# Performance work log

Hardware: AMD Instinct MI355X
Metric: run time of the kernel (lower is better)

The kernel has to match this reference:

```python
import jax, jax.numpy as jnp
import numpy as np

MIN_, MAX_, KSZ, IGNORE_IDX = 10, 10, 3, -255
B, H, W = 256, 256, 256
LI_MAX_ITERS = 64


def setup_inputs() -> dict:
    key = jax.random.key(0)
    x = jax.random.uniform(key, (B, 1, H, W), dtype=jnp.float32)
    return {"x": x}


def _otsu(hist):
    # hist: [256] counts. Returns Otsu threshold (bin value); fg = img > t.
    bins = jnp.arange(256, dtype=jnp.float32)
    w0 = jnp.cumsum(hist)[:-1]
    w1 = hist.sum() - w0
    s0 = jnp.cumsum(hist * bins)[:-1]
    s_tot = (hist * bins).sum()
    m0 = s0 / jnp.maximum(w0, 1e-12)
    m1 = (s_tot - s0) / jnp.maximum(w1, 1e-12)
    var_b = w0 * w1 * (m0 - m1) ** 2
    return jnp.argmax(var_b).astype(jnp.float32)


def _li(hist, init_t):
    # Histogram-based Li iterative minimum cross-entropy threshold
    # (skimage.filters.threshold_li with initial_guess=init_t).
    bins = jnp.arange(256, dtype=jnp.float32)
    img_min = jnp.min(jnp.where(hist > 0, bins, 255.0))
    vals = bins - img_min  # shift so values >= 0 (as skimage does)
    csum = jnp.cumsum(hist)
    cvsum = jnp.cumsum(hist * vals)
    n_tot, s_tot = csum[-1], cvsum[-1]
    tol = 0.5  # integer image -> half the minimal value spacing

    def body(state):
        t_curr, _, i = state
        # background: img <= t_curr + img_min
        idx = jnp.clip(jnp.floor(t_curr + img_min).astype(jnp.int32), 0, 255)
        n_back, s_back = csum[idx], cvsum[idx]
        n_fore, s_fore = n_tot - n_back, s_tot - s_back
        mean_back = jnp.where(n_back > 0, s_back / jnp.maximum(n_back, 1.0), 0.0)
        mean_fore = s_fore / jnp.maximum(n_fore, 1.0)
        eps = 1e-12
        t_next = (mean_back - mean_fore) / (
            jnp.log(jnp.maximum(mean_back, eps)) - jnp.log(jnp.maximum(mean_fore, eps)))
        t_next = jnp.where(mean_back < eps, mean_fore / 2.0, t_next)
        return (t_next, t_curr, i + 1)

    def cond(state):
        t_curr, t_prev, i = state
        return (jnp.abs(t_curr - t_prev) > tol) & (i < LI_MAX_ITERS)

    t0 = init_t - img_min
    t_fin, _, _ = jax.lax.while_loop(cond, body, (t0, t0 + 10.0, 0))
    return t_fin + img_min


def _sample_mask(key, region, k):
    # Uniform sampling without replacement of up to k pixels from region
    # (bool [H,W]) via random-score top-k (equiv. to torch.multinomial
    # with uniform probs, w/o replacement).
    flat = region.reshape(-1)
    scores = jnp.where(flat, jax.random.uniform(key, (flat.shape[0],)), -1.0)
    top, idx = jax.lax.top_k(scores, k)
    valid = (top >= 0.0).astype(jnp.int32)
    mask = jnp.zeros(flat.shape[0], jnp.int32).at[idx].max(valid)
    return mask.reshape(region.shape)


def _dilate(m):
    # kornia dilation with ones (KSZ,KSZ) kernel on a 0/1 mask == max filter.
    return jax.lax.reduce_window(m, 0, jax.lax.max, (KSZ, KSZ), (1, 1), "SAME")


def _per_image(img_u8, key_fg, key_bg):
    # img_u8: [H,W] int32 in [0,255]
    hist = jnp.zeros(256, jnp.float32).at[img_u8.ravel()].add(1.0)
    otsu = jnp.clip(_otsu(hist), 1.0, 254.0)  # clamp 0->1, 255->254
    li_t = _li(hist, otsu)
    roi = img_u8.astype(jnp.float32) > li_t

    fg = _sample_mask(key_fg, roi, MAX_)
    bg = _sample_mask(key_bg, jnp.logical_not(roi), MIN_)
    if KSZ > 1:
        fg = _dilate(fg)
        bg = _dilate(bg)

    overlap = (fg + bg) == 2
    fg = jnp.where(overlap, 0, fg)
    bg = jnp.where(overlap, 0, bg)

    seeds = jnp.full((H, W), IGNORE_IDX, jnp.int32)
    seeds = jnp.where(bg == 1, 0, seeds)
    seeds = jnp.where(fg == 1, 1, seeds)
    return seeds


def reference(x):
    b = x.shape[0]
    # (cam*255).astype(uint8): truncation, cam in [0,1]
    img = jnp.clip(jnp.floor(x[:, 0] * 255.0), 0, 255).astype(jnp.int32)
    keys = jax.random.split(jax.random.key(1), (b, 2))
    return jax.vmap(_per_image)(img, keys[:, 0], keys[:, 1])
```

## Files before the change

kernel.cpp:

```cpp
#include <hip/hip_runtime.h>
#include <stdint.h>

#define NPIX 65536
#define IGN (-255)
#define CAP 1022
#define META_LI   2048
#define META_CF   2049
#define META_CB   2050
#define META_NROI 2051
#define META_FG   2052
#define META_BG   3074

__device__ __forceinline__ uint32_t rotl32(uint32_t v, uint32_t r){ return (v<<r)|(v>>(32u-r)); }

__device__ __forceinline__ void tf2x32(uint32_t k0, uint32_t k1, uint32_t x0, uint32_t x1,
                                       uint32_t &o0, uint32_t &o1){
  uint32_t k2 = k0 ^ k1 ^ 0x1BD11BDAu;
  x0 += k0; x1 += k1;
#define TFR(r) { x0 += x1; x1 = rotl32(x1,(r)); x1 ^= x0; }
  TFR(13u) TFR(15u) TFR(26u) TFR(6u)   x0 += k1; x1 += k2 + 1u;
  TFR(17u) TFR(29u) TFR(16u) TFR(24u)  x0 += k2; x1 += k0 + 2u;
  TFR(13u) TFR(15u) TFR(26u) TFR(6u)   x0 += k0; x1 += k1 + 3u;
  TFR(17u) TFR(29u) TFR(16u) TFR(24u)  x0 += k1; x1 += k2 + 4u;
  TFR(13u) TFR(15u) TFR(26u) TFR(6u)   x0 += k2; x1 += k0 + 5u;
#undef TFR
  o0 = x0; o1 = x1;
}

__device__ __forceinline__ unsigned long long packCand(uint32_t bits, uint32_t pix){
  float f = __uint_as_float((bits >> 9) | 0x3f800000u) - 1.0f;
  uint32_t u = __float_as_uint(f) ^ 0x80000000u;
  return ((unsigned long long)u << 32) | (unsigned long long)(0xFFFFFFFFu - pix);
}

__device__ __forceinline__ void t10_insert(unsigned long long* l, unsigned long long c){
  if (c > l[9]) {
    l[9] = c;
#pragma unroll
    for (int i = 9; i > 0; --i){
      unsigned long long a = l[i-1], b2 = l[i];
      if (b2 > a){ l[i-1] = b2; l[i] = a; }
    }
  }
}

__global__ __launch_bounds__(256, 8)
void ka_hist_fill(const float* __restrict__ x, int* __restrict__ out){
  const int blk = blockIdx.x;
  const int b = blk >> 3, j8 = blk & 7;
  const int tid = threadIdx.x;
  const float4* x4 = (const float4*)(x + (size_t)b * NPIX) + j8 * 2048;
  int4* o4 = (int4*)(out + (size_t)b * NPIX) + j8 * 2048;

  __shared__ uint32_t histR[1024];
#pragma unroll
  for (int k = 0; k < 4; ++k) histR[tid + 256*k] = 0u;
  __syncthreads();

  const int4 f4 = make_int4(IGN, IGN, IGN, IGN);
  const uint32_t c4 = (uint32_t)(tid & 3);
#pragma unroll
  for (int jj = 0; jj < 8; ++jj){
    int p4 = tid + 256*jj;
    float4 v = x4[p4];
    if (j8 != 0 || jj >= 4) o4[p4] = f4;
    uint32_t u0 = (uint32_t)min(max((int)floorf(v.x*255.0f),0),255);
    uint32_t u1 = (uint32_t)min(max((int)floorf(v.y*255.0f),0),255);
    uint32_t u2 = (uint32_t)min(max((int)floorf(v.z*255.0f),0),255);
    uint32_t u3 = (uint32_t)min(max((int)floorf(v.w*255.0f),0),255);
    atomicAdd(&histR[(u0<<2)|c4],1u); atomicAdd(&histR[(u1<<2)|c4],1u);
    atomicAdd(&histR[(u2<<2)|c4],1u); atomicAdd(&histR[(u3<<2)|c4],1u);
  }
  __syncthreads();
  uint32_t s = histR[4*tid] + histR[4*tid+1] + histR[4*tid+2] + histR[4*tid+3];
  out[(size_t)b*NPIX + j8*256 + tid] = (int)s;
}

__global__ __launch_bounds__(256, 2)
void kb_thresh(int* __restrict__ out){
  const int b = blockIdx.x;
  const int tid = threadIdx.x;
  int* meta = out + (size_t)b * NPIX;

  __shared__ float csum[256], cvsum[256];
  __shared__ int s_imin;
  __shared__ unsigned long long s_best;
  if (tid == 0){ s_imin = 255; s_best = 0ull; }
  __syncthreads();

  int h = 0;
#pragma unroll
  for (int j = 0; j < 8; ++j) h += meta[j*256 + tid];
  if (h) atomicMin(&s_imin, tid);
  __syncthreads();
  const float img_min = (float)s_imin;

  csum[tid]  = (float)h;
  cvsum[tid] = (float)h * ((float)tid - img_min);
  __syncthreads();
  for (int off = 1; off < 256; off <<= 1){
    float a = 0.f, c2 = 0.f;
    if (tid >= off){ a = csum[tid-off]; c2 = cvsum[tid-off]; }
    __syncthreads();
    if (tid >= off){ csum[tid] += a; cvsum[tid] += c2; }
    __syncthreads();
  }

  {
    float s_tot_o = cvsum[255] + img_min * csum[255];
    if (tid < 255){
      float w0 = csum[tid];
      float w1 = 65536.0f - w0;
      float cs = cvsum[tid] + img_min * csum[tid];
      float m0 = cs / fmaxf(w0, 1e-12f);
      float m1 = (s_tot_o - cs) / fmaxf(w1, 1e-12f);
      float d = m0 - m1;
      float vb = (w0*w1) * (d*d);
      unsigned long long pk =
        ((unsigned long long)__float_as_uint(vb) << 32) | (unsigned long long)(255 - tid);
      atomicMax(&s_best, pk);
    }
  }
  __syncthreads();

  if (tid == 0){
    int bestIdx = 255 - (int)(s_best & 0xFFFFFFFFull);
    float otsu = fminf(fmaxf((float)bestIdx, 1.0f), 254.0f);
    float n_tot = csum[255], s_tot = cvsum[255];
    float t_curr = otsu - img_min, t_prev = t_curr + 10.0f;
    int it = 0;
    while (fabsf(t_curr - t_prev) > 0.5f && it < 64){
      int idx = min(max((int)floorf(t_curr + img_min), 0), 255);
      float n_back = csum[idx], s_back = cvsum[idx];
      float n_fore = n_tot - n_back, s_fore = s_tot - s_back;
      float mean_back = (n_back > 0.0f) ? (s_back / fmaxf(n_back, 1.0f)) : 0.0f;
      float mean_fore = s_fore / fmaxf(n_fore, 1.0f);
      float t_next = (mean_back - mean_fore) /
                     (logf(fmaxf(mean_back, 1e-12f)) - logf(fmaxf(mean_fore, 1e-12f)));
      if (mean_back < 1e-12f) t_next = mean_fore * 0.5f;
      t_prev = t_curr; t_curr = t_next; ++it;
    }
    float lit = t_curr + img_min;
    meta[META_LI] = __float_as_int(lit);
    int idx = min(max((int)floorf(lit), 0), 255);
    meta[META_NROI] = NPIX - (int)csum[idx];
    meta[META_CF] = 0;
    meta[META_CB] = 0;
  }
}

__global__ __launch_bounds__(256, 4)
void kc_score(const float* __restrict__ x, int* __restrict__ out){
  const int blk = blockIdx.x;
  const int b = blk >> 3, j8 = blk & 7;
  const int tid = threadIdx.x;
  int* meta = out + (size_t)b * NPIX;
  const float4* x4 = (const float4*)(x + (size_t)b * NPIX) + j8 * 2048;

  __shared__ uint32_t s_kw[4];
  __shared__ float s_lit;
  if (tid < 2){
    uint32_t o0, o1;
    tf2x32(0u, 1u, 0u, (uint32_t)(2*b + tid), o0, o1);
    s_kw[2*tid] = o0; s_kw[2*tid+1] = o1;
  }
  if (tid == 0) s_lit = __int_as_float(meta[META_LI]);
  __syncthreads();

  const float lit = s_lit;
  const uint32_t fk0 = s_kw[0], fk1 = s_kw[1], bk0 = s_kw[2], bk1 = s_kw[3];
  const uint32_t THRM = (0xFF000000u >> 9);
#pragma unroll
  for (int jj = 0; jj < 8; ++jj){
    int p4 = tid + 256*jj;
    float4 v = x4[p4];
    uint32_t u0 = (uint32_t)min(max((int)floorf(v.x*255.0f),0),255);
    uint32_t u1 = (uint32_t)min(max((int)floorf(v.y*255.0f),0),255);
    uint32_t u2 = (uint32_t)min(max((int)floorf(v.z*255.0f),0),255);
    uint32_t u3 = (uint32_t)min(max((int)floorf(v.w*255.0f),0),255);
    uint32_t pk = u0 | (u1<<8) | (u2<<16) | (u3<<24);
    uint32_t pix0 = (uint32_t)(j8*8192 + 4*p4);
#pragma unroll
    for (int s = 0; s < 4; ++s){
      uint32_t q = (pk >> (8*s)) & 255u;
      bool r = ((float)q > lit);
      uint32_t o0, o1;
      tf2x32(r ? fk0 : bk0, r ? fk1 : bk1, 0u, pix0 + (uint32_t)s, o0, o1);
      uint32_t bits = o0 ^ o1;
      if ((bits >> 9) >= THRM){
        int r2 = r ? 0 : 1;
        int idx = atomicAdd(&meta[META_CF + r2], 1);
        if (idx < CAP) meta[(r2 ? META_BG : META_FG) + idx] = (int)(pix0 + (uint32_t)s);
      }
    }
  }
}

__global__ __launch_bounds__(1024, 4)
void kd_final(const float* __restrict__ x, int* __restrict__ out){
  const int b = blockIdx.x;
  const int tid = threadIdx.x;
  int* meta = out + (size_t)b * NPIX;
  int* outb = meta;
  const float* img = x + (size_t)b * NPIX;

  __shared__ unsigned long long buf[2][CAP];
  __shared__ uint32_t s_kw[4];
  __shared__ int s_cnt[2], s_fail[2], s_np[2];
  __shared__ float s_lit;
  __shared__ int s_pr[2][10], s_pc[2][10];

  if (tid < 2){
    uint32_t o0, o1;
    tf2x32(0u, 1u, 0u, (uint32_t)(2*b + tid), o0, o1);
    s_kw[2*tid] = o0; s_kw[2*tid+1] = o1;
  }
  if (tid == 0){
    s_lit = __int_as_float(meta[META_LI]);
    int c0 = meta[META_CF], c1 = meta[META_CB];
    int nroi = meta[META_NROI];
    s_cnt[0] = c0; s_cnt[1] = c1;
    int m0r = nroi, m1r = NPIX - nroi;
    s_fail[0] = (c0 > CAP) || (c0 < 10 && c0 != m0r);
    s_fail[1] = (c1 > CAP) || (c1 < 10 && c1 != m1r);
  }
  __syncthreads();

  {
    int r2 = tid >> 9, lane = tid & 511;
    uint32_t kk0 = s_kw[2*r2], kk1 = s_kw[2*r2+1];
    int n = min(s_cnt[r2], CAP);
    for (int i = lane; i < n; i += 512){
      uint32_t pix = (uint32_t)meta[(r2 ? META_BG : META_FG) + i];
      uint32_t o0, o1; tf2x32(kk0, kk1, 0u, pix, o0, o1);
      buf[r2][i] = packCand(o0 ^ o1, pix);
    }
  }
  __syncthreads();

  const float lit = s_lit;
  if (s_fail[0] || s_fail[1]){
    if (tid < 64){
      for (int r2 = 0; r2 < 2; ++r2){
        if (!s_fail[r2]) continue;
        uint32_t kk0 = s_kw[2*r2], kk1 = s_kw[2*r2+1];
        unsigned long long t[10];
#pragma unroll
        for (int i = 0; i < 10; ++i) t[i] = 0ull;
        for (int k2 = 0; k2 < 1024; ++k2){
          uint32_t pix = (uint32_t)(tid + 64*k2);
          float v = img[pix];
          int q = min(max((int)floorf(v*255.0f),0),255);
          bool r = ((float)q > lit);
          if (r != (r2 == 0)) continue;
          uint32_t o0, o1; tf2x32(kk0, kk1, 0u, pix, o0, o1);
          t10_insert(t, packCand(o0 ^ o1, pix));
        }
#pragma unroll
        for (int i = 0; i < 10; ++i) buf[r2][tid*10 + i] = t[i];
      }
    }
    __syncthreads();
    if (tid < 2 && s_fail[tid]){
      unsigned long long t[10];
#pragma unroll
      for (int i = 0; i < 10; ++i) t[i] = 0ull;
      for (int i = 0; i < 640; ++i) t10_insert(t, buf[tid][i]);
#pragma unroll
      for (int i = 0; i < 10; ++i) buf[tid][i] = t[i];
      s_cnt[tid] = 10;
    }
    __syncthreads();
  }

  if (tid == 0 || tid == 64){
    int r2 = (tid == 0) ? 0 : 1;
    int n = min(s_cnt[r2], CAP);
    unsigned long long t[10];
#pragma unroll
    for (int i = 0; i < 10; ++i) t[i] = 0ull;
    for (int i = 0; i < n; ++i) t10_insert(t, buf[r2][i]);
    int np = 0;
    for (int i = 0; i < 10; ++i){
      if (t[i]){
        uint32_t pix = 0xFFFFFFFFu - (uint32_t)(t[i] & 0xFFFFFFFFull);
        s_pr[r2][np] = (int)(pix >> 8);
        s_pc[r2][np] = (int)(pix & 255u);
        ++np;
      }
    }
    s_np[r2] = np;
  }
  __syncthreads();

  ((int4*)meta)[tid] = make_int4(IGN, IGN, IGN, IGN);
  __syncthreads();

  const int nfg = s_np[0], nbg = s_np[1];
  const int npts = nfg + nbg;
  if (tid < npts*9){
    int k = tid / 9, d = tid - k*9;
    int pr = (k < nfg) ? s_pr[0][k] : s_pr[1][k - nfg];
    int pc = (k < nfg) ? s_pc[0][k] : s_pc[1][k - nfg];
    pr += d/3 - 1; pc += d%3 - 1;
    if (pr >= 0 && pr < 256 && pc >= 0 && pc < 256){
      bool fgd = false, bgd = false;
      for (int i = 0; i < nfg; ++i) fgd |= (abs(pr - s_pr[0][i]) <= 1) && (abs(pc - s_pc[0][i]) <= 1);
      for (int i = 0; i < nbg; ++i) bgd |= (abs(pr - s_pr[1][i]) <= 1) && (abs(pc - s_pc[1][i]) <= 1);
      int val = (fgd && bgd) ? IGN : (fgd ? 1 : 0);
      outb[pr*256 + pc] = val;
    }
  }
}

extern "C" void kernel_launch(void* const* d_in, const int* in_sizes, int n_in,
                              void* d_out, int out_size, void* d_ws, size_t ws_size,
                              hipStream_t stream) {
  const float* x = (const float*)d_in[0];
  int* out = (int*)d_out;
  int B = in_sizes[0] / NPIX;
  ka_hist_fill<<<8*B, 256, 0, stream>>>(x, out);
  kb_thresh  <<<B,   256, 0, stream>>>(out);
  kc_score   <<<8*B, 256, 0, stream>>>(x, out);
  kd_final   <<<B,  1024, 0, stream>>>(x, out);
}
```

Measured before the change: 193.7 us.

## Cache packed uint8 image in output scratch and reuse it in scoring kernels

The histogram kernel now quantizes each pixel once and stores the 8-bit values, packed four per int, in the first quarter of each image's output buffer. The scoring and fallback paths then read this compact copy instead of re-reading and re-quantizing the float input. The Li threshold is turned into an integer cutoff, so pixel classification becomes a plain integer compare. The metadata and scratch layout are moved so the packed image fits, and the final kernel now clears a larger region of the output to overwrite that scratch.

```diff
diff --git a/kernel.cpp b/kernel.cpp
--- a/kernel.cpp
+++ b/kernel.cpp
@@ -4,12 +4,15 @@
 #define NPIX 65536
 #define IGN (-255)
 #define CAP 1022
-#define META_LI   2048
-#define META_CF   2049
-#define META_CB   2050
-#define META_NROI 2051
-#define META_FG   2052
-#define META_BG   3074
+#define U8N    16384
+#define HPART  16384
+#define M_THR  18432
+#define M_CF   18433
+#define M_CB   18434
+#define M_NROI 18435
+#define M_FG   18436
+#define M_BG   19458
+#define SCR_I4 5120
 
 __device__ __forceinline__ uint32_t rotl32(uint32_t v, uint32_t r){ return (v<<r)|(v>>(32u-r)); }
 
@@ -49,8 +52,9 @@
   const int blk = blockIdx.x;
   const int b = blk >> 3, j8 = blk & 7;
   const int tid = threadIdx.x;
-  const float4* x4 = (const float4*)(x + (size_t)b * NPIX) + j8 * 2048;
-  int4* o4 = (int4*)(out + (size_t)b * NPIX) + j8 * 2048;
+  const float4* x4 = (const float4*)(x + (size_t)b * NPIX);
+  int* base = out + (size_t)b * NPIX;
+  int4* o4 = (int4*)base;
 
   __shared__ uint32_t histR[1024];
 #pragma unroll
@@ -61,19 +65,20 @@
   const uint32_t c4 = (uint32_t)(tid & 3);
 #pragma unroll
   for (int jj = 0; jj < 8; ++jj){
-    int p4 = tid + 256*jj;
-    float4 v = x4[p4];
-    if (j8 != 0 || jj >= 4) o4[p4] = f4;
+    int i4 = j8*2048 + jj*256 + tid;
+    float4 v = x4[i4];
     uint32_t u0 = (uint32_t)min(max((int)floorf(v.x*255.0f),0),255);
     uint32_t u1 = (uint32_t)min(max((int)floorf(v.y*255.0f),0),255);
     uint32_t u2 = (uint32_t)min(max((int)floorf(v.z*255.0f),0),255);
     uint32_t u3 = (uint32_t)min(max((int)floorf(v.w*255.0f),0),255);
+    base[i4] = (int)(u0 | (u1<<8) | (u2<<16) | (u3<<24));
+    if (i4 >= SCR_I4) o4[i4] = f4;
     atomicAdd(&histR[(u0<<2)|c4],1u); atomicAdd(&histR[(u1<<2)|c4],1u);
     atomicAdd(&histR[(u2<<2)|c4],1u); atomicAdd(&histR[(u3<<2)|c4],1u);
   }
   __syncthreads();
   uint32_t s = histR[4*tid] + histR[4*tid+1] + histR[4*tid+2] + histR[4*tid+3];
-  out[(size_t)b*NPIX + j8*256 + tid] = (int)s;
+  base[HPART + j8*256 + tid] = (int)s;
 }
 
 __global__ __launch_bounds__(256, 2)
@@ -90,7 +95,7 @@
 
   int h = 0;
 #pragma unroll
-  for (int j = 0; j < 8; ++j) h += meta[j*256 + tid];
+  for (int j = 0; j < 8; ++j) h += meta[HPART + j*256 + tid];
   if (h) atomicMin(&s_imin, tid);
   __syncthreads();
   const float img_min = (float)s_imin;
@@ -141,73 +146,79 @@
       t_prev = t_curr; t_curr = t_next; ++it;
     }
     float lit = t_curr + img_min;
-    meta[META_LI] = __float_as_int(lit);
-    int idx = min(max((int)floorf(lit), 0), 255);
-    meta[META_NROI] = NPIX - (int)csum[idx];
-    meta[META_CF] = 0;
-    meta[META_CB] = 0;
-  }
-}
-
-__global__ __launch_bounds__(256, 4)
-void kc_score(const float* __restrict__ x, int* __restrict__ out){
+    int qthr;
+    if (!(lit == lit)) qthr = 256;
+    else               qthr = (int)floorf(lit) + 1;
+    meta[M_THR] = qthr;
+    int nlo = (qthr <= 0) ? 0 : (int)csum[min(qthr, 256) - 1];
+    meta[M_NROI] = NPIX - nlo;
+    meta[M_CF] = 0;
+    meta[M_CB] = 0;
+  }
+}
+
+__global__ __launch_bounds__(256, 8)
+void kc_score(int* __restrict__ out){
   const int blk = blockIdx.x;
   const int b = blk >> 3, j8 = blk & 7;
   const int tid = threadIdx.x;
   int* meta = out + (size_t)b * NPIX;
-  const float4* x4 = (const float4*)(x + (size_t)b * NPIX) + j8 * 2048;
+  const int4* u4 = (const int4*)meta;
 
   __shared__ uint32_t s_kw[4];
-  __shared__ float s_lit;
+  __shared__ int s_thr;
   if (tid < 2){
     uint32_t o0, o1;
     tf2x32(0u, 1u, 0u, (uint32_t)(2*b + tid), o0, o1);
     s_kw[2*tid] = o0; s_kw[2*tid+1] = o1;
   }
-  if (tid == 0) s_lit = __int_as_float(meta[META_LI]);
-  __syncthreads();
-
-  const float lit = s_lit;
+  if (tid == 0) s_thr = meta[M_THR];
+  __syncthreads();
+
+  const int qthr = s_thr;
   const uint32_t fk0 = s_kw[0], fk1 = s_kw[1], bk0 = s_kw[2], bk1 = s_kw[3];
   const uint32_t THRM = (0xFF000000u >> 9);
-#pragma unroll
-  for (int jj = 0; jj < 8; ++jj){
-    int p4 = tid + 256*jj;
-    float4 v = x4[p4];
-    uint32_t u0 = (uint32_t)min(max((int)floorf(v.x*255.0f),0),255);
-    uint32_t u1 = (uint32_t)min(max((int)floorf(v.y*255.0f),0),255);
-    uint32_t u2 = (uint32_t)min(max((int)floorf(v.z*255.0f),0),255);
-    uint32_t u3 = (uint32_t)min(max((int)floorf(v.w*255.0f),0),255);
-    uint32_t pk = u0 | (u1<<8) | (u2<<16) | (u3<<24);
-    uint32_t pix0 = (uint32_t)(j8*8192 + 4*p4);
-#pragma unroll
-    for (int s = 0; s < 4; ++s){
-      uint32_t q = (pk >> (8*s)) & 255u;
-      bool r = ((float)q > lit);
-      uint32_t o0, o1;
-      tf2x32(r ? fk0 : bk0, r ? fk1 : bk1, 0u, pix0 + (uint32_t)s, o0, o1);
-      uint32_t bits = o0 ^ o1;
-      if ((bits >> 9) >= THRM){
-        int r2 = r ? 0 : 1;
-        int idx = atomicAdd(&meta[META_CF + r2], 1);
-        if (idx < CAP) meta[(r2 ? META_BG : META_FG) + idx] = (int)(pix0 + (uint32_t)s);
+  int4 w0 = u4[j8*512 + tid];
+  int4 w1 = u4[j8*512 + 256 + tid];
+  const uint32_t pixA = (uint32_t)(j8*8192 + 16*tid);
+  const uint32_t pixB = (uint32_t)(j8*8192 + 4096 + 16*tid);
+#pragma unroll
+  for (int half = 0; half < 2; ++half){
+    int4 w = half ? w1 : w0;
+    uint32_t pb = half ? pixB : pixA;
+    const uint32_t words[4] = {(uint32_t)w.x,(uint32_t)w.y,(uint32_t)w.z,(uint32_t)w.w};
+#pragma unroll
+    for (int m = 0; m < 4; ++m){
+      uint32_t pk = words[m];
+#pragma unroll
+      for (int s = 0; s < 4; ++s){
+        int q = (int)((pk >> (8*s)) & 255u);
+        bool r = (q >= qthr);
+        uint32_t pix = pb + (uint32_t)(4*m + s);
+        uint32_t o0, o1;
+        tf2x32(r ? fk0 : bk0, r ? fk1 : bk1, 0u, pix, o0, o1);
+        uint32_t bits = o0 ^ o1;
+        if ((bits >> 9) >= THRM){
+          int r2 = r ? 0 : 1;
+          int idx = atomicAdd(&meta[M_CF + r2], 1);
+          if (idx < CAP) meta[(r2 ? M_BG : M_FG) + idx] = (int)pix;
+        }
       }
     }
   }
 }
 
 __global__ __launch_bounds__(1024, 4)
-void kd_final(const float* __restrict__ x, int* __restrict__ out){
+void kd_final(int* __restrict__ out){
   const int b = blockIdx.x;
   const int tid = threadIdx.x;
   int* meta = out + (size_t)b * NPIX;
   int* outb = meta;
-  const float* img = x + (size_t)b * NPIX;
 
   __shared__ unsigned long long buf[2][CAP];
   __shared__ uint32_t s_kw[4];
   __shared__ int s_cnt[2], s_fail[2], s_np[2];
-  __shared__ float s_lit;
+  __shared__ int s_thr;
   __shared__ int s_pr[2][10], s_pc[2][10];
 
   if (tid < 2){
@@ -216,9 +227,9 @@
     s_kw[2*tid] = o0; s_kw[2*tid+1] = o1;
   }
   if (tid == 0){
-    s_lit = __int_as_float(meta[META_LI]);
-    int c0 = meta[META_CF], c1 = meta[META_CB];
-    int nroi = meta[META_NROI];
+    s_thr = meta[M_THR];
+    int c0 = meta[M_CF], c1 = meta[M_CB];
+    int nroi = meta[M_NROI];
     s_cnt[0] = c0; s_cnt[1] = c1;
     int m0r = nroi, m1r = NPIX - nroi;
     s_fail[0] = (c0 > CAP) || (c0 < 10 && c0 != m0r);
@@ -231,14 +242,14 @@
     uint32_t kk0 = s_kw[2*r2], kk1 = s_kw[2*r2+1];
     int n = min(s_cnt[r2], CAP);
     for (int i = lane; i < n; i += 512){
-      uint32_t pix = (uint32_t)meta[(r2 ? META_BG : META_FG) + i];
+      uint32_t pix = (uint32_t)meta[(r2 ? M_BG : M_FG) + i];
       uint32_t o0, o1; tf2x32(kk0, kk1, 0u, pix, o0, o1);
       buf[r2][i] = packCand(o0 ^ o1, pix);
     }
   }
   __syncthreads();
 
-  const float lit = s_lit;
+  const int qthr = s_thr;
   if (s_fail[0] || s_fail[1]){
     if (tid < 64){
       for (int r2 = 0; r2 < 2; ++r2){
@@ -249,9 +260,8 @@
         for (int i = 0; i < 10; ++i) t[i] = 0ull;
         for (int k2 = 0; k2 < 1024; ++k2){
           uint32_t pix = (uint32_t)(tid + 64*k2);
-          float v = img[pix];
-          int q = min(max((int)floorf(v*255.0f),0),255);
-          bool r = ((float)q > lit);
+          int q = (int)(((uint32_t)meta[pix >> 2] >> (8*(pix & 3u))) & 255u);
+          bool r = (q >= qthr);
           if (r != (r2 == 0)) continue;
           uint32_t o0, o1; tf2x32(kk0, kk1, 0u, pix, o0, o1);
           t10_insert(t, packCand(o0 ^ o1, pix));
@@ -293,7 +303,9 @@
   }
   __syncthreads();
 
-  ((int4*)meta)[tid] = make_int4(IGN, IGN, IGN, IGN);
+#pragma unroll
+  for (int k = 0; k < 5; ++k)
+    ((int4*)meta)[tid*5 + k] = make_int4(IGN, IGN, IGN, IGN);
   __syncthreads();
 
   const int nfg = s_np[0], nbg = s_np[1];
@@ -321,6 +333,6 @@
   int B = in_sizes[0] / NPIX;
   ka_hist_fill<<<8*B, 256, 0, stream>>>(x, out);
   kb_thresh  <<<B,   256, 0, stream>>>(out);
-  kc_score   <<<8*B, 256, 0, stream>>>(x, out);
-  kd_final   <<<B,  1024, 0, stream>>>(x, out);
-}
+  kc_score   <<<8*B, 256, 0, stream>>>(out);
+  kd_final   <<<B,  1024, 0, stream>>>(out);
+}
```

Result: no change. 196.6 us (+1.5%).
